# Kernel optimization log

Hardware: AMD Instinct MI355X
Metric: run time of the kernel (lower is better)

Reference implementation:

```python
import jax, jax.numpy as jnp
import numpy as np

STRIDE = 1


def setup_inputs() -> dict:
    key = jax.random.key(0)
    ks = jax.random.split(key, 8)
    B, m, C, H, W = 4, 4096, 256, 384, 384
    return {
        "original_kpts": jax.random.uniform(ks[0], (B, m, 2), dtype=jnp.float32),
        "segment": jax.random.normal(ks[1], (B, C, H, W), dtype=jnp.float32),
        "conv_w": jax.random.normal(ks[2], (9,), dtype=jnp.float32),
        "conv_b": jax.random.normal(ks[3], (1,), dtype=jnp.float32),
        "lin_w": jax.random.normal(ks[4], (1, C), dtype=jnp.float32),
        "lin_b": jax.random.normal(ks[5], (1,), dtype=jnp.float32),
        "ca_w1": jax.random.normal(ks[6], (C, C), dtype=jnp.float32),
        "ca_w2": jax.random.normal(ks[7], (C, C), dtype=jnp.float32),
    }


def reference(original_kpts, segment, conv_w, conv_b, lin_w, lin_b, ca_w1, ca_w2):
    B, C, H, W = segment.shape
    m = original_kpts.shape[1]
    # integer pixel coords per keypoint: (m, B)
    x = jnp.floor(original_kpts[:, :, 0].T * H).astype(jnp.int32)
    y = jnp.floor(original_kpts[:, :, 1].T * W).astype(jnp.int32)
    offs = jnp.array([-STRIDE, 0, STRIDE], dtype=jnp.int32)
    dx, dy = jnp.meshgrid(offs, offs, indexing="ij")
    dx, dy = dx.reshape(-1), dy.reshape(-1)  # (9,)
    xo = jnp.clip(x[:, :, None] + dx, 0, H - 1)  # (m, B, 9)
    yo = jnp.clip(y[:, :, None] + dy, 0, W - 1)
    # flat spatial indices; permute(0,2,1).reshape(-1,B) as in the original (m-major, 9-minor)
    idx = (xo * W + yo).transpose(0, 2, 1).reshape(-1, B)  # (9m, B)
    # gather 9 neighboring pixels per keypoint per batch
    fseg = segment.reshape(B, C, H * W)  # (B, C, HW)
    idx_b = jnp.broadcast_to(idx.T[:, None, :], (B, C, idx.shape[0]))
    sp = jnp.take_along_axis(fseg, idx_b, axis=2)  # (B, C, 9m)
    # match torch layout: (9m, C, B) -> reshape(9, m, B, C) -> permute(0,3,2,1)
    sp = sp.transpose(2, 1, 0).reshape(9, m, B, C).transpose(0, 3, 2, 1)  # (9, C, B, m)
    # 1x1 conv over the 9 "patch" channels: input (B, 9, m, C) -> (B, m, C)
    pool = jnp.einsum("bkmc,k->bmc", sp.transpose(2, 0, 3, 1), conv_w) + conv_b[0]
    # center pixel (index 4 of the scrambled layout), (B, m, C)
    center = sp[4].transpose(1, 2, 0)
    # per-keypoint confidence: Linear(C -> 1)
    confidence = center @ lin_w.T + lin_b  # (B, m, 1)
    # CBAM-style channel attention on segment, reduction=1 -> (B, 1, C)
    avg = segment.mean(axis=(2, 3))  # (B, C)
    mx = segment.max(axis=(2, 3))  # (B, C)
    mlp = lambda v: jax.nn.relu(v @ ca_w1.T) @ ca_w2.T
    s = jax.nn.sigmoid(mlp(avg) + mlp(mx))[:, None, :]  # (B, 1, C)
    return (1.0 - confidence) * pool + center + s  # (B, m, C)
```

## Files before the change

kernel.cpp:

```cpp
#include <hip/hip_runtime.h>
#include <math.h>

#define Mm 4096
#define Cc 256
#define Hh 384
#define Ww 384
#define HW (Hh * Ww)

__global__ __launch_bounds__(256) void k3_scan_gather(
    const float* __restrict__ kpts, const float* __restrict__ seg,
    const float* __restrict__ conv_w, const float* __restrict__ conv_b,
    float* __restrict__ pool_ws, float* __restrict__ cent_ws,
    float* __restrict__ avg_ws, float* __restrict__ max_ws)
{
    const int p = blockIdx.x;
    const int b  = p & 3;
    const int cc = p >> 2;
    const int t  = threadIdx.x;

    const float* plane = seg + (size_t)(b * Cc + cc) * HW;

    __shared__ short2 sxy[Mm];
    __shared__ float red[16];

    const float* kb = kpts + (size_t)b * Mm * 2;
    for (int i = t; i < Mm; i += 256) {
        float kx = kb[2 * i];
        float ky = kb[2 * i + 1];
        short xi = (short)floorf(kx * (float)Hh);
        short yi = (short)floorf(ky * (float)Ww);
        sxy[i] = make_short2(xi, yi);
    }

    const float4* plane4 = (const float4*)plane;
    float lsum = 0.0f, lmax = -INFINITY;
    for (int idx = t; idx < HW / 4; idx += 256) {
        float4 v = plane4[idx];
        lsum += (v.x + v.y) + (v.z + v.w);
        lmax = fmaxf(lmax, fmaxf(fmaxf(v.x, v.y), fmaxf(v.z, v.w)));
    }
    #pragma unroll
    for (int off = 32; off > 0; off >>= 1) {
        lsum += __shfl_down(lsum, off);
        lmax = fmaxf(lmax, __shfl_down(lmax, off));
    }
    const int wave = t >> 6;
    if ((t & 63) == 0) { red[wave] = lsum; red[8 + wave] = lmax; }
    __syncthreads();
    if (t == 0) {
        float s  = ((red[0] + red[1]) + (red[2] + red[3]));
        float mx = fmaxf(fmaxf(red[8], red[9]), fmaxf(red[10], red[11]));
        avg_ws[b * Cc + cc] = s * (1.0f / (float)HW);
        max_ws[b * Cc + cc] = mx;
    }

    float cw[9];
    #pragma unroll
    for (int k = 0; k < 9; ++k) cw[k] = conv_w[k];
    const float cb = conv_b[0];

    float* pool_col = pool_ws + (size_t)p * Mm;
    float* cent_col = cent_ws + (size_t)p * Mm;

    for (int ip = t; ip < Mm; ip += 256) {
        float pool = cb;
        float center = 0.0f;
        #pragma unroll
        for (int kp = 0; kp < 9; ++kp) {
            int j = (kp << 12) + ip;
            int i = j / 9;
            int k = j - i * 9;
            short2 xy = sxy[i];
            int dx = (k / 3) - 1;
            int dy = (k - (k / 3) * 3) - 1;
            int xo = xy.x + dx;
            int yo = xy.y + dy;
            xo = min(max(xo, 0), Hh - 1);
            yo = min(max(yo, 0), Ww - 1);
            float v = plane[xo * Ww + yo];
            pool = fmaf(cw[kp], v, pool);
            if (kp == 4) center = v;
        }
        pool_col[ip] = pool;
        cent_col[ip] = center;
    }
}

__global__ __launch_bounds__(256) void k2_mlp(
    const float* __restrict__ avg_ws, const float* __restrict__ max_ws,
    const float* __restrict__ w1, const float* __restrict__ w2,
    float* __restrict__ s_ws)
{
    const int bb = blockIdx.x;
    const int t  = threadIdx.x;
    __shared__ float va[Cc], vm[Cc], g[Cc];
    va[t] = avg_ws[bb * Cc + t];
    vm[t] = max_ws[bb * Cc + t];
    __syncthreads();
    float ha = 0.0f, hm = 0.0f;
    const float* w1r = w1 + (size_t)t * Cc;
    for (int c = 0; c < Cc; ++c) {
        float w = w1r[c];
        ha = fmaf(w, va[c], ha);
        hm = fmaf(w, vm[c], hm);
    }
    g[t] = fmaxf(ha, 0.0f) + fmaxf(hm, 0.0f);
    __syncthreads();
    float o = 0.0f;
    const float* w2r = w2 + (size_t)t * Cc;
    for (int c = 0; c < Cc; ++c) o = fmaf(w2r[c], g[c], o);
    s_ws[bb * Cc + t] = 1.0f / (1.0f + expf(-o));
}

__global__ __launch_bounds__(256) void k4_final(
    const float* __restrict__ pool_ws, const float* __restrict__ cent_ws,
    const float* __restrict__ lin_w, const float* __restrict__ lin_b,
    const float* __restrict__ s_ws, float* __restrict__ out)
{
    const int bb = blockIdx.y;
    const int i0 = blockIdx.x * 16;
    const int t  = threadIdx.x;
    __shared__ float tp[Cc][17];
    __shared__ float tc[Cc][17];
    __shared__ float conf[16];

    const int r  = t & 15;
    const int cg = t >> 4;

    for (int pass = 0; pass < 16; ++pass) {
        int cp = pass * 16 + cg;
        size_t gidx = (size_t)(bb * Cc + cp) * Mm + i0 + r;
        tp[cp][r] = pool_ws[gidx];
        tc[cp][r] = cent_ws[gidx];
    }
    if (t < 16) conf[t] = 0.0f;
    __syncthreads();

    float part = 0.0f;
    #pragma unroll
    for (int it = 0; it < 16; ++it) {
        int cp = it * 16 + cg;
        part = fmaf(tc[cp][r], lin_w[cp], part);
    }
    atomicAdd(&conf[r], part);
    __syncthreads();

    const float lb = lin_b[0];
    for (int pass = 0; pass < 16; ++pass) {
        int rr = t >> 4;
        int cp = pass * 16 + (t & 15);
        float cf = conf[rr] + lb;
        float val = (1.0f - cf) * tp[cp][rr] + tc[cp][rr] + s_ws[bb * Cc + cp];
        out[(size_t)(bb * Mm + i0 + rr) * Cc + cp] = val;
    }
}

extern "C" void kernel_launch(void* const* d_in, const int* in_sizes, int n_in,
                              void* d_out, int out_size, void* d_ws, size_t ws_size,
                              hipStream_t stream) {
    const float* kpts   = (const float*)d_in[0];
    const float* seg    = (const float*)d_in[1];
    const float* conv_w = (const float*)d_in[2];
    const float* conv_b = (const float*)d_in[3];
    const float* lin_w  = (const float*)d_in[4];
    const float* lin_b  = (const float*)d_in[5];
    const float* w1     = (const float*)d_in[6];
    const float* w2     = (const float*)d_in[7];
    float* out = (float*)d_out;

    float* ws      = (float*)d_ws;
    float* pool_ws = ws;
    float* cent_ws = ws + (size_t)1024 * Mm;
    float* avg_ws  = ws + (size_t)2 * 1024 * Mm;
    float* max_ws  = avg_ws + 1024;
    float* s_ws    = avg_ws + 2048;

    hipLaunchKernelGGL(k3_scan_gather, dim3(1024), dim3(256), 0, stream,
                       kpts, seg, conv_w, conv_b, pool_ws, cent_ws, avg_ws, max_ws);
    hipLaunchKernelGGL(k2_mlp, dim3(4), dim3(256), 0, stream,
                       avg_ws, max_ws, w1, w2, s_ws);
    hipLaunchKernelGGL(k4_final, dim3(Mm / 16, 4), dim3(256), 0, stream,
                       pool_ws, cent_ws, lin_w, lin_b, s_ws, out);
}
```

Before: 1.002 ms.

## Bucket gather taps by row and interleave gathers with plane scan

Adds a pre-pass kernel that sorts the 9 taps of every keypoint into per-row buckets, recording pixel index and destination slot. The main kernel then scans each plane in 32-row chunks and gathers only the taps that fall in the chunk just streamed, so gather reads should hit cache instead of issuing scattered DRAM accesses. Gathered values are staged in 144 KB of LDS and the 1x1 conv is applied afterwards. The cost is an extra launch, bucket workspace traffic, and very high LDS usage, which allows only one block per CU and so lowers occupancy.

```diff
diff --git a/kernel.cpp b/kernel.cpp
--- a/kernel.cpp
+++ b/kernel.cpp
@@ -6,39 +6,103 @@
 #define Hh 384
 #define Ww 384
 #define HW (Hh * Ww)
-
-__global__ __launch_bounds__(256) void k3_scan_gather(
-    const float* __restrict__ kpts, const float* __restrict__ seg,
+#define NTAP (Mm * 9)
+
+__global__ __launch_bounds__(384) void k_buckets(
+    const float* __restrict__ kpts,
+    unsigned int* __restrict__ pix_ws,
+    unsigned short* __restrict__ vidx_ws,
+    int* __restrict__ row_start_ws)
+{
+    const int b = blockIdx.x;
+    const int t = threadIdx.x;
+    __shared__ int cnt[Hh];
+    __shared__ int offs[Hh + 1];
+    __shared__ int cur[Hh];
+
+    cnt[t] = 0;
+    __syncthreads();
+
+    const float* kb = kpts + (size_t)b * Mm * 2;
+    for (int i = t; i < Mm; i += 384) {
+        int xi = (int)floorf(kb[2 * i] * (float)Hh);
+        #pragma unroll
+        for (int dx = -1; dx <= 1; ++dx) {
+            int xo = min(max(xi + dx, 0), Hh - 1);
+            atomicAdd(&cnt[xo], 3);
+        }
+    }
+    __syncthreads();
+
+    for (int d = 1; d < Hh; d <<= 1) {
+        int add = (t >= d) ? cnt[t - d] : 0;
+        __syncthreads();
+        cnt[t] += add;
+        __syncthreads();
+    }
+    offs[t + 1] = cnt[t];
+    if (t == 0) offs[0] = 0;
+    __syncthreads();
+    cur[t] = offs[t];
+    row_start_ws[b * 385 + t] = offs[t];
+    if (t == 383) row_start_ws[b * 385 + 384] = offs[384];
+    __syncthreads();
+
+    for (int i = t; i < Mm; i += 384) {
+        int xi = (int)floorf(kb[2 * i] * (float)Hh);
+        int yi = (int)floorf(kb[2 * i + 1] * (float)Ww);
+        #pragma unroll
+        for (int k = 0; k < 9; ++k) {
+            int xo = min(max(xi + (k / 3) - 1, 0), Hh - 1);
+            int yo = min(max(yi + (k % 3) - 1, 0), Ww - 1);
+            int pos = atomicAdd(&cur[xo], 1);
+            pix_ws[(size_t)b * NTAP + pos] = (unsigned int)(xo * Ww + yo);
+            vidx_ws[(size_t)b * NTAP + pos] = (unsigned short)(i * 9 + k);
+        }
+    }
+}
+
+__global__ __launch_bounds__(256) void k3_gather(
+    const float* __restrict__ seg,
     const float* __restrict__ conv_w, const float* __restrict__ conv_b,
+    const unsigned int* __restrict__ pix_ws,
+    const unsigned short* __restrict__ vidx_ws,
+    const int* __restrict__ row_start_ws,
     float* __restrict__ pool_ws, float* __restrict__ cent_ws,
     float* __restrict__ avg_ws, float* __restrict__ max_ws)
 {
+    __shared__ float V[NTAP];
+    __shared__ float red[16];
+
     const int p = blockIdx.x;
-    const int b  = p & 3;
+    const int b = p & 3;
     const int cc = p >> 2;
-    const int t  = threadIdx.x;
+    const int t = threadIdx.x;
 
     const float* plane = seg + (size_t)(b * Cc + cc) * HW;
-
-    __shared__ short2 sxy[Mm];
-    __shared__ float red[16];
-
-    const float* kb = kpts + (size_t)b * Mm * 2;
-    for (int i = t; i < Mm; i += 256) {
-        float kx = kb[2 * i];
-        float ky = kb[2 * i + 1];
-        short xi = (short)floorf(kx * (float)Hh);
-        short yi = (short)floorf(ky * (float)Ww);
-        sxy[i] = make_short2(xi, yi);
-    }
-
-    const float4* plane4 = (const float4*)plane;
+    const unsigned int* pix = pix_ws + (size_t)b * NTAP;
+    const unsigned short* vix = vidx_ws + (size_t)b * NTAP;
+    const int* rs = row_start_ws + b * 385;
+
     float lsum = 0.0f, lmax = -INFINITY;
-    for (int idx = t; idx < HW / 4; idx += 256) {
-        float4 v = plane4[idx];
-        lsum += (v.x + v.y) + (v.z + v.w);
-        lmax = fmaxf(lmax, fmaxf(fmaxf(v.x, v.y), fmaxf(v.z, v.w)));
-    }
+
+    for (int ch = 0; ch < 12; ++ch) {
+        const float4* base = (const float4*)(plane + (size_t)ch * 32 * Ww);
+        float4 v[12];
+        #pragma unroll
+        for (int u = 0; u < 12; ++u) v[u] = base[t + 256 * u];
+        #pragma unroll
+        for (int u = 0; u < 12; ++u) {
+            lsum += (v[u].x + v[u].y) + (v[u].z + v[u].w);
+            lmax = fmaxf(lmax, fmaxf(fmaxf(v[u].x, v[u].y), fmaxf(v[u].z, v[u].w)));
+        }
+        int e0 = rs[ch * 32];
+        int e1 = rs[ch * 32 + 32];
+        for (int e = e0 + t; e < e1; e += 256) {
+            V[vix[e]] = plane[pix[e]];
+        }
+    }
+
     #pragma unroll
     for (int off = 32; off > 0; off >>= 1) {
         lsum += __shfl_down(lsum, off);
@@ -61,28 +125,13 @@
 
     float* pool_col = pool_ws + (size_t)p * Mm;
     float* cent_col = cent_ws + (size_t)p * Mm;
-
-    for (int ip = t; ip < Mm; ip += 256) {
+    for (int i2 = t; i2 < Mm; i2 += 256) {
         float pool = cb;
-        float center = 0.0f;
-        #pragma unroll
-        for (int kp = 0; kp < 9; ++kp) {
-            int j = (kp << 12) + ip;
-            int i = j / 9;
-            int k = j - i * 9;
-            short2 xy = sxy[i];
-            int dx = (k / 3) - 1;
-            int dy = (k - (k / 3) * 3) - 1;
-            int xo = xy.x + dx;
-            int yo = xy.y + dy;
-            xo = min(max(xo, 0), Hh - 1);
-            yo = min(max(yo, 0), Ww - 1);
-            float v = plane[xo * Ww + yo];
-            pool = fmaf(cw[kp], v, pool);
-            if (kp == 4) center = v;
-        }
-        pool_col[ip] = pool;
-        cent_col[ip] = center;
+        #pragma unroll
+        for (int kp = 0; kp < 9; ++kp)
+            pool = fmaf(cw[kp], V[kp * Mm + i2], pool);
+        pool_col[i2] = pool;
+        cent_col[i2] = V[4 * Mm + i2];
     }
 }
 
@@ -168,15 +217,21 @@
     const float* w2     = (const float*)d_in[7];
     float* out = (float*)d_out;
 
-    float* ws      = (float*)d_ws;
-    float* pool_ws = ws;
-    float* cent_ws = ws + (size_t)1024 * Mm;
-    float* avg_ws  = ws + (size_t)2 * 1024 * Mm;
-    float* max_ws  = avg_ws + 1024;
-    float* s_ws    = avg_ws + 2048;
-
-    hipLaunchKernelGGL(k3_scan_gather, dim3(1024), dim3(256), 0, stream,
-                       kpts, seg, conv_w, conv_b, pool_ws, cent_ws, avg_ws, max_ws);
+    char* ws = (char*)d_ws;
+    float* pool_ws = (float*)ws;                                   ws += (size_t)1024 * Mm * 4;
+    float* cent_ws = (float*)ws;                                   ws += (size_t)1024 * Mm * 4;
+    float* avg_ws  = (float*)ws;                                   ws += 1024 * 4;
+    float* max_ws  = (float*)ws;                                   ws += 1024 * 4;
+    float* s_ws    = (float*)ws;                                   ws += 1024 * 4;
+    unsigned int*   pix_ws  = (unsigned int*)ws;                   ws += (size_t)4 * NTAP * 4;
+    unsigned short* vidx_ws = (unsigned short*)ws;                 ws += (size_t)4 * NTAP * 2;
+    int* row_start_ws = (int*)ws;
+
+    hipLaunchKernelGGL(k_buckets, dim3(4), dim3(384), 0, stream,
+                       kpts, pix_ws, vidx_ws, row_start_ws);
+    hipLaunchKernelGGL(k3_gather, dim3(1024), dim3(256), 0, stream,
+                       seg, conv_w, conv_b, pix_ws, vidx_ws, row_start_ws,
+                       pool_ws, cent_ws, avg_ws, max_ws);
     hipLaunchKernelGGL(k2_mlp, dim3(4), dim3(256), 0, stream,
                        avg_ws, max_ws, w1, w2, s_ws);
     hipLaunchKernelGGL(k4_final, dim3(Mm / 16, 4), dim3(256), 0, stream,
```

Measured after the change: 915.3 us. 1.09x faster.
